# Performance work log

Measured on AMD Instinct MI355X. Metric: run time of the kernel, lower is better.

Reference implementation:

```python
import jax, jax.numpy as jnp
import numpy as np
import math

# ---- static configuration (mirrors Renderer defaults) ----
S = 129                                 # density cube side
L = math.ceil(S * math.sqrt(3))         # padded/rotation cube side = 224
C_ABS = 0.2                             # absorption coefficient c
LIGHTS = [
    {'dir': (2, 1, 1),    'rgb': (1.0, 69.0 / 255.0, 25.0 / 255.0)},
    {'dir': (-1, 0.5, 0), 'rgb': (227.0 / 255.0, 1.0, 66.0 / 255.0)},
]


def yp_from_light(l):
    ld = np.asarray(l, dtype=np.float64)
    ld = ld / np.sqrt(np.sum(ld ** 2))
    y = -math.asin(ld[0])
    if ld[2] < 0:
        y = -math.pi - y
    y = y * 180.0 / math.pi
    p = math.asin(ld[1]) * 180.0 / math.pi
    return y, p


def rot_matrix(yaw_deg, pitch_deg, order):
    # yaw about the y (height) axis, pitch about the x axis, roll = 0
    y = math.radians(yaw_deg)
    p = math.radians(pitch_deg)
    Ry = np.array([[math.cos(y), 0.0, math.sin(y)],
                   [0.0, 1.0, 0.0],
                   [-math.sin(y), 0.0, math.cos(y)]], dtype=np.float32)
    Rp = np.array([[1.0, 0.0, 0.0],
                   [0.0, math.cos(p), -math.sin(p)],
                   [0.0, math.sin(p), math.cos(p)]], dtype=np.float32)
    return Ry @ Rp if order == 'ypr' else Rp @ Ry

# base normalized sampling grid (align_corners=True convention), (x,y,z) order
_lin = np.linspace(-1.0, 1.0, L, dtype=np.float32)
_zz, _yy, _xx = np.meshgrid(_lin, _lin, _lin, indexing='ij')
BASE_XYZ = np.stack([_xx, _yy, _zz], axis=-1)   # [L,L,L,3]


def rotate_volume(vol, R):
    """Trilinear resampling of vol [B,C,D,H,W] under rotation R (zero padding)."""
    B, Ch, D, H, W = vol.shape
    src = jnp.einsum('dhwc,kc->dhwk', jnp.asarray(BASE_XYZ), jnp.asarray(R))
    xs = (src[..., 0] + 1.0) * 0.5 * (W - 1)
    ys = (src[..., 1] + 1.0) * 0.5 * (H - 1)
    zs = (src[..., 2] + 1.0) * 0.5 * (D - 1)
    x0 = jnp.floor(xs).astype(jnp.int32)
    y0 = jnp.floor(ys).astype(jnp.int32)
    z0 = jnp.floor(zs).astype(jnp.int32)
    wx = (xs - x0).astype(vol.dtype)
    wy = (ys - y0).astype(vol.dtype)
    wz = (zs - z0).astype(vol.dtype)
    flat = vol.reshape(B, Ch, D * H * W)

    def gather(zi, yi, xi):
        inb = ((zi >= 0) & (zi < D) & (yi >= 0) & (yi < H) & (xi >= 0) & (xi < W)).astype(vol.dtype)
        idx = ((jnp.clip(zi, 0, D - 1) * H + jnp.clip(yi, 0, H - 1)) * W
               + jnp.clip(xi, 0, W - 1)).reshape(-1)
        return jnp.take(flat, idx, axis=2).reshape(B, Ch, D, H, W) * inb

    out = (gather(z0,     y0,     x0)     * ((1 - wz) * (1 - wy) * (1 - wx))
         + gather(z0,     y0,     x0 + 1) * ((1 - wz) * (1 - wy) * wx)
         + gather(z0,     y0 + 1, x0)     * ((1 - wz) * wy * (1 - wx))
         + gather(z0,     y0 + 1, x0 + 1) * ((1 - wz) * wy * wx)
         + gather(z0 + 1, y0,     x0)     * (wz * (1 - wy) * (1 - wx))
         + gather(z0 + 1, y0,     x0 + 1) * (wz * (1 - wy) * wx)
         + gather(z0 + 1, y0 + 1, x0)     * (wz * wy * (1 - wx))
         + gather(z0 + 1, y0 + 1, x0 + 1) * (wz * wy * wx))
    return out


def _revcumsum(a):
    # torch.flip(cumsum(flip(a,[2]),2),[2]) : reverse cumulative sum along depth
    return jnp.flip(jnp.cumsum(jnp.flip(a, 2), axis=2), 2)


def setup_inputs() -> dict:
    key = jax.random.key(0)
    d = jax.random.uniform(key, (1, 1, S, S, S), dtype=jnp.float32)
    return {'d': d}


def reference(d):
    bs, _, Sd, _, _ = d.shape
    i = L // 2 - Sd // 2
    j = i + Sd
    light_array = jnp.zeros((bs, 3, Sd, Sd, Sd), dtype=d.dtype)
    for l in LIGHTS:
        y, p = yp_from_light(l['dir'])
        up = jnp.zeros((bs, 1, L, L, L), dtype=d.dtype).at[:, :, i:j, i:j, i:j].set(d)
        up = rotate_volume(up, rot_matrix(y, p, 'ypr'))
        up = jnp.exp(-C_ABS * _revcumsum(up))           # transmittance toward light
        up = rotate_volume(up, rot_matrix(-y, -p, 'rpy'))
        color = jnp.asarray(l['rgb'], dtype=d.dtype).reshape(1, 3, 1, 1, 1)
        light_array = light_array + up[:, :, i:j, i:j, i:j] * color
    t = jnp.exp(-C_ABS * _revcumsum(d))                  # view-ray transmittance
    out = C_ABS * jnp.sum(d * light_array * t, axis=2)   # background = 0
    return jnp.clip(out, 0.0, 1.0)
```

## Files before the change

### kernel.cpp

```cpp
#include <hip/hip_runtime.h>
#include <hip/hip_fp16.h>
#include <math.h>

#ifndef M_PI
#define M_PI 3.14159265358979323846
#endif

#define SS   129
#define LL   224
#define LL2  (LL*LL)
#define LL3  (LL*LL*LL)
#define SS2  (SS*SS)
#define SS3  (SS*SS*SS)
#define CABS 0.2f
#define PAD  48

#define BLO 45.5f
#define BHI 178.5f

#define NT1  28
#define NTZ16 14
#define ROTG  (2 * NTZ16 * 784)
#define ROTCH 392
#define NT3  17
#define NBZ16 9
#define BACKG (2 * NBZ16 * 289)
#define BACKCH 17
#define BACKG_P 5304
#define NTZ  28

#define NSEG 16
#define SEGZ 9
#define DSEGT (NSEG * SS2)
#define PREB1 ((DSEGT + 255) / 256)
#define PRERUNB 7
#define N4   (SS3 / 4)
#define CVT4B ((N4 + 1 + 255) / 256)
#define PREG (PREB1 + PRERUNB + CVT4B)
#define SUFG (392 + PREB1)
#define TEXPB (2 * NTZ * LL2 / 256)

#define RBX 21
#define RBY 16
#define RBZ 18
#define RBN (RBX*RBY*RBZ)
#define RSXZ (RBX*RBZ)

#define BBX 21
#define BBY 16
#define BBZ 19
#define BBN (BBX*BBY*BBZ)
#define BSXZ (BBX*BBZ)

struct Mat3 { float m[9]; };
struct F3   { float x, y, z; };

__device__ __forceinline__ F3 tile_center(const Mat3& M, int ox, int oy, int oz) {
    float cbx = fmaf((float)ox + 3.5f, 2.0f / 223.0f, -1.0f);
    float cby = fmaf((float)oy + 3.5f, 2.0f / 223.0f, -1.0f);
    float cbz = fmaf((float)oz + 3.5f, 2.0f / 223.0f, -1.0f);
    F3 qc;
    qc.x = fmaf(fmaf(M.m[0], cbx, fmaf(M.m[1], cby, M.m[2] * cbz)), 111.5f, 111.5f);
    qc.y = fmaf(fmaf(M.m[3], cbx, fmaf(M.m[4], cby, M.m[5] * cbz)), 111.5f, 111.5f);
    qc.z = fmaf(fmaf(M.m[6], cbx, fmaf(M.m[7], cby, M.m[8] * cbz)), 111.5f, 111.5f);
    return qc;
}

__device__ __forceinline__ F3 tile_center16(const Mat3& M, int ox, int oy, int oz) {
    float cbx = fmaf((float)ox + 3.5f, 2.0f / 223.0f, -1.0f);
    float cby = fmaf((float)oy + 3.5f, 2.0f / 223.0f, -1.0f);
    float cbz = fmaf((float)oz + 7.5f, 2.0f / 223.0f, -1.0f);
    F3 qc;
    qc.x = fmaf(fmaf(M.m[0], cbx, fmaf(M.m[1], cby, M.m[2] * cbz)), 111.5f, 111.5f);
    qc.y = fmaf(fmaf(M.m[3], cbx, fmaf(M.m[4], cby, M.m[5] * cbz)), 111.5f, 111.5f);
    qc.z = fmaf(fmaf(M.m[6], cbx, fmaf(M.m[7], cby, M.m[8] * cbz)), 111.5f, 111.5f);
    return qc;
}

__device__ __forceinline__ bool tile_accept(F3 qc, F3 H) {
    return !(qc.x + H.x < BLO || qc.x - H.x > BHI ||
             qc.y + H.y < BLO || qc.y - H.y > BHI ||
             qc.z + H.z < BLO || qc.z - H.z > BHI);
}

__device__ __forceinline__ void qmap(const Mat3& M, int x, int y, int z,
                                     float& qx, float& qy, float& qz) {
    float bx = fmaf((float)x, 2.0f / 223.0f, -1.0f);
    float by = fmaf((float)y, 2.0f / 223.0f, -1.0f);
    float bz = fmaf((float)z, 2.0f / 223.0f, -1.0f);
    qx = fmaf(fmaf(M.m[0], bx, fmaf(M.m[1], by, M.m[2] * bz)), 111.5f, 111.5f);
    qy = fmaf(fmaf(M.m[3], bx, fmaf(M.m[4], by, M.m[5] * bz)), 111.5f, 111.5f);
    qz = fmaf(fmaf(M.m[6], bx, fmaf(M.m[7], by, M.m[8] * bz)), 111.5f, 111.5f);
}

__device__ __forceinline__ float fetch_d(const float* __restrict__ d, int z, int y, int x) {
    unsigned zz = (unsigned)(z - PAD), yy = (unsigned)(y - PAD), xx = (unsigned)(x - PAD);
    return (zz < (unsigned)SS && yy < (unsigned)SS && xx < (unsigned)SS)
        ? d[((int)zz * SS + (int)yy) * SS + (int)xx] : 0.0f;
}

__device__ __forceinline__ float fetch_d16(const __half* __restrict__ d, int z, int y, int x) {
    unsigned zz = (unsigned)(z - PAD), yy = (unsigned)(y - PAD), xx = (unsigned)(x - PAD);
    return (zz < (unsigned)SS && yy < (unsigned)SS && xx < (unsigned)SS)
        ? __half2float(d[((int)zz * SS + (int)yy) * SS + (int)xx]) : 0.0f;
}

__device__ __forceinline__ float fetch_T(const float* __restrict__ T, int z, int y, int x) {
    unsigned zz = (unsigned)z, yy = (unsigned)y, xx = (unsigned)x;
    return (zz < (unsigned)LL && yy < (unsigned)LL && xx < (unsigned)LL)
        ? T[((int)zz * LL + (int)yy) * LL + (int)xx] : 0.0f;
}

__device__ __forceinline__ float tri_T(const float* __restrict__ T, float qz, float qy, float qx) {
    int x0 = (int)floorf(qx), y0 = (int)floorf(qy), z0 = (int)floorf(qz);
    float wx = qx - (float)x0, wy = qy - (float)y0, wz = qz - (float)z0;
    float c000 = fetch_T(T, z0, y0, x0),     c001 = fetch_T(T, z0, y0, x0 + 1);
    float c010 = fetch_T(T, z0, y0 + 1, x0), c011 = fetch_T(T, z0, y0 + 1, x0 + 1);
    float c100 = fetch_T(T, z0 + 1, y0, x0),     c101 = fetch_T(T, z0 + 1, y0, x0 + 1);
    float c110 = fetch_T(T, z0 + 1, y0 + 1, x0), c111 = fetch_T(T, z0 + 1, y0 + 1, x0 + 1);
    float a00 = c000 + wx * (c001 - c000), a01 = c010 + wx * (c011 - c010);
    float a10 = c100 + wx * (c101 - c100), a11 = c110 + wx * (c111 - c110);
    float b0 = a00 + wy * (a01 - a00), b1 = a10 + wy * (a11 - a10);
    return b0 + wz * (b1 - b0);
}

__device__ __forceinline__ float tri_d_g(const float* __restrict__ d, float qz, float qy, float qx) {
    int x0 = (int)floorf(qx), y0 = (int)floorf(qy), z0 = (int)floorf(qz);
    float wx = qx - (float)x0, wy = qy - (float)y0, wz = qz - (float)z0;
    float c000 = fetch_d(d, z0, y0, x0),     c001 = fetch_d(d, z0, y0, x0 + 1);
    float c010 = fetch_d(d, z0, y0 + 1, x0), c011 = fetch_d(d, z0, y0 + 1, x0 + 1);
    float c100 = fetch_d(d, z0 + 1, y0, x0),     c101 = fetch_d(d, z0 + 1, y0, x0 + 1);
    float c110 = fetch_d(d, z0 + 1, y0 + 1, x0), c111 = fetch_d(d, z0 + 1, y0 + 1, x0 + 1);
    float a00 = c000 + wx * (c001 - c000), a01 = c010 + wx * (c011 - c010);
    float a10 = c100 + wx * (c101 - c100), a11 = c110 + wx * (c111 - c110);
    float b0 = a00 + wy * (a01 - a00), b1 = a10 + wy * (a11 - a10);
    return b0 + wz * (b1 - b0);
}

__device__ __forceinline__ float tri_rot(const float* __restrict__ S,
                                         float qx, float qy, float qz,
                                         int lox, int loy, int loz) {
    int x0 = (int)floorf(qx), y0 = (int)floorf(qy), z0 = (int)floorf(qz);
    float wx = qx - (float)x0, wy = qy - (float)y0, wz = qz - (float)z0;
    int i = (y0 - loy) * 378 + (z0 - loz) * 21 + (x0 - lox);
    float c000 = S[i],        c001 = S[i + 1];
    float cz0  = S[i + 21],   cz1  = S[i + 22];
    float cy0  = S[i + 378],  cy1  = S[i + 379];
    float cw0  = S[i + 399],  cw1  = S[i + 400];
    float a00 = c000 + wx * (c001 - c000);
    float a01 = cy0  + wx * (cy1  - cy0);
    float a10 = cz0  + wx * (cz1  - cz0);
    float a11 = cw0  + wx * (cw1  - cw0);
    float b0  = a00 + wy * (a01 - a00);
    float b1  = a10 + wy * (a11 - a10);
    return b0 + wz * (b1 - b0);
}

__device__ __forceinline__ float tri_back(const float* __restrict__ S,
                                          float qx, float qy, float qz,
                                          int lox, int loy, int loz) {
    int x0 = (int)floorf(qx), y0 = (int)floorf(qy), z0 = (int)floorf(qz);
    float wx = qx - (float)x0, wy = qy - (float)y0, wz = qz - (float)z0;
    int i = (y0 - loy) * 399 + (z0 - loz) * 21 + (x0 - lox);
    float c000 = S[i],        c001 = S[i + 1];
    float cz0  = S[i + 21],   cz1  = S[i + 22];
    float cy0  = S[i + 399],  cy1  = S[i + 400];
    float cw0  = S[i + 420],  cw1  = S[i + 421];
    float a00 = c000 + wx * (c001 - c000);
    float a01 = cy0  + wx * (cy1  - cy0);
    float a10 = cz0  + wx * (cz1  - cz0);
    float a11 = cw0  + wx * (cw1  - cw0);
    float b0  = a00 + wy * (a01 - a00);
    float b1  = a10 + wy * (a11 - a10);
    return b0 + wz * (b1 - b0);
}

__global__ __launch_bounds__(256) void k_pre(const float* __restrict__ d,
        float* __restrict__ Dseg, float* __restrict__ A,
        unsigned short* __restrict__ Run, __half* __restrict__ d16,
        Mat3 M0, Mat3 M1, F3 H0, F3 H1) {
    int b = blockIdx.x;
    if (b < PREB1) {
        int t = b * 256 + threadIdx.x;
        if (t < 2 * SS2) A[t] = 0.0f;
        if (t >= DSEGT) return;
        int seg = t / SS2, col = t - seg * SS2;
        int zs = seg * SEGZ, ze = min(SS, zs + SEGZ);
        float run = 0.0f;
        for (int z = zs; z < ze; ++z) run += d[z * SS2 + col];
        Dseg[t] = run;
    } else if (b < PREB1 + PRERUNB) {
        int id = (b - PREB1) * 256 + threadIdx.x;
        if (id >= 2 * 784) return;
        int l = id / 784, r = id - l * 784;
        int ty = r / 28, tx = r - ty * 28;
        const Mat3 M = l ? M1 : M0;
        const F3  H  = l ? H1 : H0;
        int t0 = -1, t1 = -1;
        for (int tz = 0; tz < NT1; ++tz) {
            F3 qc = tile_center(M, tx * 8, ty * 8, tz * 8);
            if (tile_accept(qc, H)) { if (t0 < 0) t0 = tz; t1 = tz; }
        }
        Run[id] = (t0 < 0) ? 0xFFFFu : (unsigned short)(t0 | (t1 << 8));
    } else {
        int t4 = (b - PREB1 - PRERUNB) * 256 + threadIdx.x;
        if (t4 < N4) {
            float4 v = ((const float4*)d)[t4];
            __half2* o = (__half2*)(d16 + 4 * t4);
            o[0] = __floats2half2_rn(v.x, v.y);
            o[1] = __floats2half2_rn(v.z, v.w);
        } else if (t4 == N4) {
            d16[SS3 - 1] = __float2half(d[SS3 - 1]);
        }
    }
}

__global__ __launch_bounds__(512) void k_rot(const __half* __restrict__ d16,
        __half* __restrict__ T0, __half* __restrict__ T1,
        float* __restrict__ S0, float* __restrict__ S1,
        const unsigned short* __restrict__ Run,
        Mat3 M0, Mat3 M1, F3 H0, F3 H1) {
    int n = blockIdx.x;
    int x8 = n & 7, i8 = n >> 3;
    int c = i8 / ROTCH, off = i8 - c * ROTCH;
    int b = (c * 8 + x8) * ROTCH + off;

    int light = b / (NTZ16 * 784);
    int r = b - light * (NTZ16 * 784);
    int tz16 = r / 784;
    int r2 = r - tz16 * 784;
    int tty = r2 / 28, ttx = r2 - tty * 28;

    unsigned short rt = Run[light * 784 + tty * 28 + ttx];
    if (rt == 0xFFFFu) return;
    int t0 = rt & 0xFF, t1 = rt >> 8;
    if (2 * tz16 + 1 < t0 || 2 * tz16 > t1) return;

    const Mat3 M = light ? M1 : M0;
    const F3  H  = light ? H1 : H0;
    __half* __restrict__ T   = light ? T1 : T0;
    float* __restrict__ Ssum = light ? S1 : S0;

    int ox = ttx * 8, oy = tty * 8, oz = tz16 * 16;
    F3 qc = tile_center16(M, ox, oy, oz);

    int lox = (int)floorf(qc.x - H.x);
    int loy = (int)floorf(qc.y - H.y);
    int loz = (int)floorf(qc.z - H.z);

    __shared__ float S[RBN];
    __shared__ float Sc[1024];
    int tid = threadIdx.x;

    if (tid < RSXZ) {
        int ix = tid % RBX, iz = tid / RBX;
        bool interior = (lox >= PAD) & (lox <= PAD + SS - RBX) &
                        (loy >= PAD) & (loy <= PAD + SS - RBY) &
                        (loz >= PAD) & (loz <= PAD + SS - RBZ);
        if (interior) {
            const __half* g = d16 + ((size_t)(loz + iz - PAD) * SS + (loy - PAD)) * SS
                                  + (lox + ix - PAD);
            #pragma unroll
            for (int j = 0; j < RBY; ++j)
                S[tid + j * RSXZ] = __half2float(g[j * SS]);
        } else {
            #pragma unroll
            for (int j = 0; j < RBY; ++j)
                S[tid + j * RSXZ] = fetch_d16(d16, loz + iz, loy + j, lox + ix);
        }
    }
    __syncthreads();

    int lx = tid & 7, ly = (tid >> 3) & 7, lz = tid >> 6;
    int col = tid & 63;
    float fx = (float)lx - 3.5f, fy = (float)ly - 3.5f, fz = (float)lz - 7.5f;
    float qx = qc.x + fmaf(M.m[0], fx, fmaf(M.m[1], fy, M.m[2] * fz));
    float qy = qc.y + fmaf(M.m[3], fx, fmaf(M.m[4], fy, M.m[5] * fz));
    float qz = qc.z + fmaf(M.m[6], fx, fmaf(M.m[7], fy, M.m[8] * fz));
    float v0 = tri_rot(S, qx, qy, qz, lox, loy, loz);
    float qx2 = qx + 8.0f * M.m[2];
    float qy2 = qy + 8.0f * M.m[5];
    float qz2 = qz + 8.0f * M.m[8];
    float v1 = tri_rot(S, qx2, qy2, qz2, lox, loy, loz);

    Sc[lz * 64 + col] = v0;
    Sc[(lz + 8) * 64 + col] = v1;
    __syncthreads();
    if (tid < 128) {
        int cc = tid & 63;
        int so = (oy + (cc >> 3)) * LL + (ox + (cc & 7));
        if (tid < 64) {
            float s = 0.0f;
            #pragma unroll
            for (int k = 15; k >= 8; --k) { s += Sc[k * 64 + cc]; Sc[k * 64 + cc] = s; }
            Ssum[(2 * tz16 + 1) * LL2 + so] = s;
        } else {
            float s2 = 0.0f;
            #pragma unroll
            for (int k = 7; k >= 0; --k) { s2 += Sc[k * 64 + cc]; Sc[k * 64 + cc] = s2; }
            Ssum[(2 * tz16) * LL2 + so] = s2;
        }
    }
    __syncthreads();
    if (tid < 128) {
        int zz = tid >> 3, ly2 = tid & 7;
        const float4* Sc4 = (const float4*)Sc;
        float4 f0 = Sc4[zz * 16 + ly2 * 2];
        float4 f1 = Sc4[zz * 16 + ly2 * 2 + 1];
        union { __half2 h[4]; float4 v; } u;
        u.h[0] = __floats2half2_rn(f0.x, f0.y);
        u.h[1] = __floats2half2_rn(f0.z, f0.w);
        u.h[2] = __floats2half2_rn(f1.x, f1.y);
        u.h[3] = __floats2half2_rn(f1.z, f1.w);
        *(float4*)&T[(size_t)(oz + zz) * LL2 + (oy + ly2) * LL + ox] = u.v;
    }
}

__global__ __launch_bounds__(256) void k_sufw(float* __restrict__ S0,
        float* __restrict__ S1, const unsigned short* __restrict__ Run,
        const float* __restrict__ d, const float* __restrict__ Dseg,
        __half* __restrict__ W) {
    int b = blockIdx.x;
    if (b < 392) {
        int l = b / 196;
        int col = (b - l * 196) * 256 + threadIdx.x;
        float* __restrict__ Ssum = l ? S1 : S0;
        int x = col % LL, y = col / LL;
        unsigned short r = Run[l * 784 + (y >> 3) * 28 + (x >> 3)];
        if (r == 0xFFFFu) return;
        int t0 = r & 0xFF, t1 = r >> 8;
        float vbuf[NTZ];
        #pragma unroll
        for (int t = 0; t < NTZ; ++t)
            vbuf[t] = (t >= t0 && t <= t1) ? Ssum[t * LL2 + col] : 0.0f;
        float run = 0.0f;
        #pragma unroll
        for (int t = NTZ - 1; t >= 0; --t) {
            if (t >= t0 && t <= t1) Ssum[t * LL2 + col] = run;
            run += vbuf[t];
        }
    } else {
        int t = (b - 392) * 256 + threadIdx.x;
        if (t >= DSEGT) return;
        int seg = t / SS2, col = t - seg * SS2;
        int zs = seg * SEGZ, ze = min(SS, zs + SEGZ);
        float run = 0.0f;
        for (int s2 = seg + 1; s2 < NSEG; ++s2) run += Dseg[s2 * SS2 + col];
        for (int z = ze - 1; z >= zs; --z) {
            float dv = d[z * SS2 + col];
            run += dv;
            W[z * SS2 + col] = __float2half(dv * __expf(-CABS * run));
        }
    }
}

__global__ __launch_bounds__(256) void k_texp(__half* __restrict__ T0,
        __half* __restrict__ T1, const float* __restrict__ S0,
        const float* __restrict__ S1, const unsigned short* __restrict__ Run) {
    int id = blockIdx.x * 256 + threadIdx.x;
    int light = id / (NTZ * LL2);
    int r = id - light * (NTZ * LL2);
    int t = r / LL2, col = r - t * LL2;
    int y = col / LL, x = col - y * LL;
    unsigned short rt = Run[light * 784 + (y >> 3) * 28 + (x >> 3)];
    if (rt == 0xFFFFu) return;
    int t0 = rt & 0xFF, t1 = rt >> 8;
    if (t < t0 || t > t1) return;
    const float* __restrict__ Ssum = light ? S1 : S0;
    __half* __restrict__ T = light ? T1 : T0;
    float off = Ssum[t * LL2 + col];
    size_t base = (size_t)(8 * t) * LL2 + col;
    #pragma unroll
    for (int k = 0; k < 8; ++k) {
        size_t idx = base + (size_t)k * LL2;
        T[idx] = __float2half(__expf(-CABS * (__half2float(T[idx]) + off)));
    }
}

template<bool BINT>
__global__ __launch_bounds__(512) void k_back(const __half* __restrict__ T0,
        const __half* __restrict__ T1, const __half* __restrict__ W,
        float* __restrict__ A0, float* __restrict__ A1,
        Mat3 M0, Mat3 M1, F3 H0, F3 H1) {
    int n = blockIdx.x;
    int x8 = n & 7, i8 = n >> 3;
    int c = i8 / BACKCH, off = i8 - c * BACKCH;
    int lb = (c * 8 + x8) * BACKCH + off;
    if (lb >= BACKG) return;

    int light = lb / (NBZ16 * 289); lb -= light * (NBZ16 * 289);
    int tz16 = lb / 289;
    int r2 = lb - tz16 * 289;
    int tty = r2 / 17, ttx = r2 - tty * 17;

    const Mat3 M = light ? M1 : M0;
    const F3  H  = light ? H1 : H0;
    const __half* __restrict__ T = light ? T1 : T0;
    float* __restrict__ A = light ? A1 : A0;

    int ox = ttx * 8, oy = tty * 8, oz = tz16 * 16;
    F3 qc = tile_center16(M, ox + PAD, oy + PAD, oz + PAD);
    int lox = (int)floorf(qc.x - H.x);
    int loy = (int)floorf(qc.y - H.y);
    int loz = (int)floorf(qc.z - H.z);

    __shared__ float S[BBN];
    __shared__ float Sc[512];
    int tid = threadIdx.x;

    if (tid < BSXZ) {
        int ix = tid % BBX, iz = tid / BBX;
        if (BINT) {
            const __half* tb = T + ((size_t)(loz + iz) * LL + loy) * LL + (lox + ix);
            #pragma unroll
            for (int j = 0; j < BBY; ++j)
                S[tid + j * BSXZ] = __half2float(tb[j * LL]);
        } else {
            #pragma unroll
            for (int j = 0; j < BBY; ++j) {
                int gz = loz + iz, gy = loy + j, gx = lox + ix;
                bool inb = ((unsigned)gz < (unsigned)LL) & ((unsigned)gy < (unsigned)LL)
                         & ((unsigned)gx < (unsigned)LL);
                S[tid + j * BSXZ] = inb
                    ? __half2float(T[((size_t)gz * LL + gy) * LL + gx]) : 0.0f;
            }
        }
    }
    __syncthreads();

    int lx = tid & 7, ly = (tid >> 3) & 7, lz = tid >> 6;
    int col = tid & 63;
    int x = ox + lx, y = oy + ly;
    float v0 = 0.0f, v1 = 0.0f;
    if (x < SS && y < SS) {
        float fx = (float)lx - 3.5f, fy = (float)ly - 3.5f, fz = (float)lz - 7.5f;
        float qx = qc.x + fmaf(M.m[0], fx, fmaf(M.m[1], fy, M.m[2] * fz));
        float qy = qc.y + fmaf(M.m[3], fx, fmaf(M.m[4], fy, M.m[5] * fz));
        float qz = qc.z + fmaf(M.m[6], fx, fmaf(M.m[7], fy, M.m[8] * fz));
        int z0 = oz + lz, z1 = oz + 8 + lz;
        if (z0 < SS)
            v0 = tri_back(S, qx, qy, qz, lox, loy, loz)
               * __half2float(W[(z0 * SS + y) * SS + x]);
        if (z1 < SS) {
            float qx2 = qx + 8.0f * M.m[2];
            float qy2 = qy + 8.0f * M.m[5];
            float qz2 = qz + 8.0f * M.m[8];
            v1 = tri_back(S, qx2, qy2, qz2, lox, loy, loz)
               * __half2float(W[(z1 * SS + y) * SS + x]);
        }
    }
    Sc[lz * 64 + col] = v0 + v1;
    __syncthreads();
    if (tid < 64) {
        float s = 0.0f;
        #pragma unroll
        for (int k = 0; k < 8; ++k) s += Sc[k * 64 + tid];
        int xx = ox + (tid & 7), yy = oy + (tid >> 3);
        if (xx < SS && yy < SS) atomicAdd(&A[yy * SS + xx], s);
    }
}

__global__ __launch_bounds__(256) void k_combine(const float* __restrict__ A0,
        const float* __restrict__ A1, float* __restrict__ out, F3 c0, F3 c1) {
    int i = blockIdx.x * 256 + threadIdx.x;
    if (i >= 3 * SS2) return;
    int ch = i / SS2, col = i - ch * SS2;
    float r0 = (ch == 0) ? c0.x : ((ch == 1) ? c0.y : c0.z);
    float r1 = (ch == 0) ? c1.x : ((ch == 1) ? c1.y : c1.z);
    float o = CABS * (A0[col] * r0 + A1[col] * r1);
    out[i] = fminf(fmaxf(o, 0.0f), 1.0f);
}

__global__ __launch_bounds__(256) void k_rot_full(const float* __restrict__ d,
                                                  float* __restrict__ T, Mat3 R) {
    int i = blockIdx.x * 256 + threadIdx.x;
    if (i >= LL3) return;
    int x = i % LL; int r = i / LL; int y = r % LL; int z = r / LL;
    float qx, qy, qz; qmap(R, x, y, z, qx, qy, qz);
    T[i] = tri_d_g(d, qz, qy, qx);
}

__global__ __launch_bounds__(256) void k_scan_full(float* __restrict__ T) {
    int col = blockIdx.x * 256 + threadIdx.x;
    if (col >= LL2) return;
    float run = 0.0f;
    for (int z = LL - 1; z >= 0; --z) {
        int idx = z * LL2 + col;
        run += T[idx];
        T[idx] = __expf(-CABS * run);
    }
}

__global__ __launch_bounds__(64) void k_fused_back(const float* __restrict__ T,
        const float* __restrict__ d, float* __restrict__ LA, Mat3 RT,
        float cr, float cg, float cb, int first) {
    int col = blockIdx.x * 64 + threadIdx.x;
    if (col >= SS2) return;
    int y = col / SS, x = col % SS;
    float run = 0.0f, acc = 0.0f;
    for (int z = SS - 1; z >= 0; --z) {
        float qx, qy, qz; qmap(RT, x + PAD, y + PAD, z + PAD, qx, qy, qz);
        float u = tri_T(T, qz, qy, qx);
        float dv = d[z * SS2 + col];
        run += dv;
        acc = fmaf(dv * __expf(-CABS * run), u, acc);
    }
    if (first) {
        LA[0 * SS2 + col] = acc * cr;
        LA[1 * SS2 + col] = acc * cg;
        LA[2 * SS2 + col] = acc * cb;
    } else {
        LA[0 * SS2 + col] += acc * cr;
        LA[1 * SS2 + col] += acc * cg;
        LA[2 * SS2 + col] += acc * cb;
    }
}

__global__ __launch_bounds__(256) void k_clip(const float* __restrict__ LA,
                                              float* __restrict__ out) {
    int i = blockIdx.x * 256 + threadIdx.x;
    if (i < 3 * SS2) out[i] = fminf(fmaxf(CABS * LA[i], 0.0f), 1.0f);
}

static void light_mats(const double ld_in[3], Mat3& R, Mat3& RT) {
    double n = sqrt(ld_in[0]*ld_in[0] + ld_in[1]*ld_in[1] + ld_in[2]*ld_in[2]);
    double l0 = ld_in[0]/n, l1 = ld_in[1]/n, l2 = ld_in[2]/n;
    double yv = -asin(l0);
    if (l2 < 0) yv = -M_PI - yv;
    double yd = yv * 180.0 / M_PI, pd = asin(l1) * 180.0 / M_PI;
    double yr = yd * M_PI / 180.0, pr = pd * M_PI / 180.0;
    float cy = (float)cos(yr), sy = (float)sin(yr), cp = (float)cos(pr), sp = (float)sin(pr);
    float m[9] = { cy,  sy*sp,  sy*cp,
                   0.f, cp,    -sp,
                  -sy,  cy*sp,  cy*cp };
    for (int i = 0; i < 9; ++i) R.m[i] = m[i];
    RT.m[0] = m[0]; RT.m[1] = m[3]; RT.m[2] = m[6];
    RT.m[3] = m[1]; RT.m[4] = m[4]; RT.m[5] = m[7];
    RT.m[6] = m[2]; RT.m[7] = m[5]; RT.m[8] = m[8];
}

static F3 half_span8(const Mat3& M) {
    F3 h;
    h.x = 3.5f * (fabsf(M.m[0]) + fabsf(M.m[1]) + fabsf(M.m[2])) + 0.05f;
    h.y = 3.5f * (fabsf(M.m[3]) + fabsf(M.m[4]) + fabsf(M.m[5])) + 0.05f;
    h.z = 3.5f * (fabsf(M.m[6]) + fabsf(M.m[7]) + fabsf(M.m[8])) + 0.05f;
    return h;
}

static F3 half_span16(const Mat3& M) {
    F3 h;
    h.x = 3.5f * (fabsf(M.m[0]) + fabsf(M.m[1])) + 7.5f * fabsf(M.m[2]) + 0.1f;
    h.y = 3.5f * (fabsf(M.m[3]) + fabsf(M.m[4])) + 7.5f * fabsf(M.m[5]) + 0.1f;
    h.z = 3.5f * (fabsf(M.m[6]) + fabsf(M.m[7])) + 7.5f * fabsf(M.m[8]) + 0.1f;
    return h;
}

static void h_qc16(const Mat3& M, double ox, double oy, double oz, double q[3]) {
    double cb[3] = { (ox + 3.5) * 2.0 / 223.0 - 1.0,
                     (oy + 3.5) * 2.0 / 223.0 - 1.0,
                     (oz + 7.5) * 2.0 / 223.0 - 1.0 };
    for (int k = 0; k < 3; ++k)
        q[k] = ((double)M.m[3*k] * cb[0] + (double)M.m[3*k+1] * cb[1]
              + (double)M.m[3*k+2] * cb[2]) * 111.5 + 111.5;
}

extern "C" void kernel_launch(void* const* d_in, const int* in_sizes, int n_in,
                              void* d_out, int out_size, void* d_ws, size_t ws_size,
                              hipStream_t stream) {
    const float* d = (const float*)d_in[0];
    float* out = (float*)d_out;

    const double dirs[2][3] = { {2.0, 1.0, 1.0}, {-1.0, 0.5, 0.0} };
    F3 c0 = { 1.0f, 69.0f / 255.0f, 25.0f / 255.0f };
    F3 c1 = { 227.0f / 255.0f, 1.0f, 66.0f / 255.0f };
    Mat3 R[2], RT[2];
    light_mats(dirs[0], R[0], RT[0]);
    light_mats(dirs[1], R[1], RT[1]);
    F3 H8[2]  = { half_span8(R[0]),  half_span8(R[1])  };
    F3 H16[2] = { half_span16(R[0]), half_span16(R[1]) };
    F3 HB[2]  = { half_span16(RT[0]), half_span16(RT[1]) };

    bool bint = true;
    for (int l = 0; l < 2 && bint; ++l) {
        double H[3] = { HB[l].x, HB[l].y, HB[l].z };
        int dim[3] = { BBX, BBY, BBZ };
        for (int tz = 0; tz < NBZ16 && bint; ++tz)
            for (int ty = 0; ty < NT3 && bint; ++ty)
                for (int tx = 0; tx < NT3; ++tx) {
                    double q[3]; h_qc16(RT[l], tx * 8 + PAD, ty * 8 + PAD, tz * 16 + PAD, q);
                    for (int k = 0; k < 3; ++k) {
                        int lo = (int)floor(q[k] - H[k]);
                        if (lo < 1 || lo + dim[k] > LL - 1) { bint = false; break; }
                    }
                    if (!bint) break;
                }
    }

    const size_t f32n = (size_t)(2 * NTZ * LL2 + NSEG * SS2 + 2 * SS2);
    const size_t need_A = f32n * 4 + (size_t)(SS3 + 2 * LL3) * 2 + 2 * 784 * 2;
    const size_t need_C = (size_t)(LL3 + 3 * SS2) * 4;

    if (ws_size >= need_A) {
        float* S0   = (float*)d_ws;
        float* S1   = S0 + NTZ * LL2;
        float* Dseg = S1 + NTZ * LL2;
        float* A0   = Dseg + NSEG * SS2;
        float* A1   = A0 + SS2;
        __half* d16 = (__half*)(A1 + SS2);
        __half* W   = d16;
        __half* T0  = d16 + SS3;
        __half* T1  = T0 + LL3;
        unsigned short* Run = (unsigned short*)(T1 + LL3);

        k_pre  <<<PREG, 256, 0, stream>>>(d, Dseg, A0, Run, d16,
                                          R[0], R[1], H8[0], H8[1]);
        k_rot  <<<ROTG, 512, 0, stream>>>(d16, T0, T1, S0, S1, Run,
                                          R[0], R[1], H16[0], H16[1]);
        k_sufw <<<SUFG, 256, 0, stream>>>(S0, S1, Run, d, Dseg, W);
        k_texp <<<TEXPB, 256, 0, stream>>>(T0, T1, S0, S1, Run);
        if (bint)
            k_back<true><<<BACKG_P, 512, 0, stream>>>(T0, T1, W, A0, A1,
                                                      RT[0], RT[1], HB[0], HB[1]);
        else
            k_back<false><<<BACKG_P, 512, 0, stream>>>(T0, T1, W, A0, A1,
                                                       RT[0], RT[1], HB[0], HB[1]);
        k_combine<<<(3 * SS2 + 255) / 256, 256, 0, stream>>>(A0, A1, out, c0, c1);
    } else if (ws_size >= need_C) {
        float* T  = (float*)d_ws;
        float* LA = T + LL3;
        for (int l = 0; l < 2; ++l) {
            k_rot_full <<<(LL3 + 255) / 256, 256, 0, stream>>>(d, T, R[l]);
            k_scan_full<<<(LL2 + 255) / 256, 256, 0, stream>>>(T);
            k_fused_back<<<(SS2 + 63) / 64, 64, 0, stream>>>(T, d, LA, RT[l],
                l ? c1.x : c0.x, l ? c1.y : c0.y, l ? c1.z : c0.z, l == 0);
        }
        k_clip<<<(3 * SS2 + 255) / 256, 256, 0, stream>>>(LA, out);
    }
}
```

Measured before the change: 169.2 us.

## Move per-segment suffix scan from rotation kernel into vectorized half2 exp kernel

The rotation kernel no longer runs an in-shared-memory suffix scan over each 8-slice segment before writing T. It now writes the raw rotated samples, and a second group of threads computes the segment totals in parallel, which drops one barrier. The exp kernel now does the within-segment reverse cumsum in registers and handles two adjacent columns per thread using half2 loads and stores, halving its thread count. Rounding changes slightly because T now holds raw fp16 samples rather than fp16 partial sums.

After: 168.2 us. No clear change (-0.6%).

```diff
diff --git a/kernel.cpp b/kernel.cpp
--- a/kernel.cpp
+++ b/kernel.cpp
@@ -38,7 +38,7 @@
 #define CVT4B ((N4 + 1 + 255) / 256)
 #define PREG (PREB1 + PRERUNB + CVT4B)
 #define SUFG (392 + PREB1)
-#define TEXPB (2 * NTZ * LL2 / 256)
+#define TEXPB (2 * NTZ * LL2 / 2 / 256)
 
 #define RBX 21
 #define RBY 16
@@ -287,22 +287,6 @@
     Sc[(lz + 8) * 64 + col] = v1;
     __syncthreads();
     if (tid < 128) {
-        int cc = tid & 63;
-        int so = (oy + (cc >> 3)) * LL + (ox + (cc & 7));
-        if (tid < 64) {
-            float s = 0.0f;
-            #pragma unroll
-            for (int k = 15; k >= 8; --k) { s += Sc[k * 64 + cc]; Sc[k * 64 + cc] = s; }
-            Ssum[(2 * tz16 + 1) * LL2 + so] = s;
-        } else {
-            float s2 = 0.0f;
-            #pragma unroll
-            for (int k = 7; k >= 0; --k) { s2 += Sc[k * 64 + cc]; Sc[k * 64 + cc] = s2; }
-            Ssum[(2 * tz16) * LL2 + so] = s2;
-        }
-    }
-    __syncthreads();
-    if (tid < 128) {
         int zz = tid >> 3, ly2 = tid & 7;
         const float4* Sc4 = (const float4*)Sc;
         float4 f0 = Sc4[zz * 16 + ly2 * 2];
@@ -313,6 +297,14 @@
         u.h[2] = __floats2half2_rn(f1.x, f1.y);
         u.h[3] = __floats2half2_rn(f1.z, f1.w);
         *(float4*)&T[(size_t)(oz + zz) * LL2 + (oy + ly2) * LL + ox] = u.v;
+    } else if (tid < 256) {
+        int t2 = tid - 128;
+        int cc = t2 & 63, h = t2 >> 6;
+        float s = 0.0f;
+        #pragma unroll
+        for (int k = 0; k < 8; ++k) s += Sc[(h * 8 + k) * 64 + cc];
+        int so = (oy + (cc >> 3)) * LL + (ox + (cc & 7));
+        Ssum[(2 * tz16 + h) * LL2 + so] = s;
     }
 }
 
@@ -358,22 +350,33 @@
         __half* __restrict__ T1, const float* __restrict__ S0,
         const float* __restrict__ S1, const unsigned short* __restrict__ Run) {
     int id = blockIdx.x * 256 + threadIdx.x;
-    int light = id / (NTZ * LL2);
-    int r = id - light * (NTZ * LL2);
-    int t = r / LL2, col = r - t * LL2;
+    int light = id / (NTZ * LL2 / 2);
+    int r = id - light * (NTZ * LL2 / 2);
+    int t = r / (LL2 / 2), cp = r - t * (LL2 / 2);
+    int col = cp * 2;
     int y = col / LL, x = col - y * LL;
-    unsigned short rt = Run[light * 784 + (y >> 3) * 28 + (x >> 3)];
-    if (rt == 0xFFFFu) return;
-    int t0 = rt & 0xFF, t1 = rt >> 8;
-    if (t < t0 || t > t1) return;
+    const unsigned short* Rl = Run + light * 784 + (y >> 3) * 28;
+    unsigned short rtA = Rl[x >> 3];
+    unsigned short rtB = Rl[(x + 1) >> 3];
+    bool aA = (rtA != 0xFFFFu) && t >= (rtA & 0xFF) && t <= (rtA >> 8);
+    bool aB = (rtB != 0xFFFFu) && t >= (rtB & 0xFF) && t <= (rtB >> 8);
+    if (!aA && !aB) return;
     const float* __restrict__ Ssum = light ? S1 : S0;
     __half* __restrict__ T = light ? T1 : T0;
-    float off = Ssum[t * LL2 + col];
-    size_t base = (size_t)(8 * t) * LL2 + col;
+    float offA = aA ? Ssum[t * LL2 + col]     : 0.0f;
+    float offB = aB ? Ssum[t * LL2 + col + 1] : 0.0f;
+    __half2* Tp = (__half2*)(T + (size_t)(8 * t) * LL2 + col);
+    float2 v[8];
+    #pragma unroll
+    for (int k = 0; k < 8; ++k) v[k] = __half22float2(Tp[k * (LL2 / 2)]);
+    float sA = 0.0f, sB = 0.0f;
+    #pragma unroll
+    for (int k = 7; k >= 0; --k) { sA += v[k].x; sB += v[k].y; v[k].x = sA; v[k].y = sB; }
     #pragma unroll
     for (int k = 0; k < 8; ++k) {
-        size_t idx = base + (size_t)k * LL2;
-        T[idx] = __float2half(__expf(-CABS * (__half2float(T[idx]) + off)));
+        float eA = aA ? __expf(-CABS * (v[k].x + offA)) : v[k].x;
+        float eB = aB ? __expf(-CABS * (v[k].y + offB)) : v[k].y;
+        Tp[k * (LL2 / 2)] = __floats2half2_rn(eA, eB);
     }
 }
 
```
